# Optimization experiments

Measured on AMD Instinct MI355X. Metric: run time of the kernel, lower is better.

The kernel has to match this reference:

```python
import jax, jax.numpy as jnp
import numpy as np

B, H, SQ, SKV, D, TOPK = 1, 16, 1024, 4096, 128, 64


def setup_inputs() -> dict:
    key = jax.random.key(0)
    kq, kk, kv, ki, ks = jax.random.split(key, 5)
    q = jax.random.normal(kq, (B, H, SQ, D), dtype=jnp.float32)
    k = jax.random.normal(kk, (B, H, SKV, D), dtype=jnp.float32)
    v = jax.random.normal(kv, (B, H, SKV, D), dtype=jnp.float32)
    topk_indices = jax.random.randint(ki, (B, SQ, TOPK), 0, SKV, dtype=jnp.int32)
    topk_scores = jax.random.uniform(ks, (B, SQ, TOPK), dtype=jnp.float32)
    return {"q": q, "k": k, "v": v, "topk_indices": topk_indices,
            "topk_scores": topk_scores}


def reference(q, k, v, topk_indices, topk_scores):
    # q: (b,h,s,d); k,v: (b,h,S,d) global (cp_world_size=1 all-gather is identity)
    head_dim = q.shape[-1]
    scale = head_dim ** -0.5
    # Gather selected K/V per query without dense (b,h,s,S,d) expansion.
    # idx: (b,1,s,topk,1) broadcast against (b,h,1,S,d) along axis=3.
    idx = topk_indices[:, None, :, :, None]
    k_g = jnp.take_along_axis(k[:, :, None, :, :], idx, axis=3)  # (b,h,s,t,d)
    v_g = jnp.take_along_axis(v[:, :, None, :, :], idx, axis=3)  # (b,h,s,t,d)
    scores = jnp.einsum("bhsd,bhstd->bhst", q, k_g) * scale
    w = jax.nn.softmax(scores, axis=-1)
    # rescale by indexer scores and renormalize
    w = w * topk_scores[:, None, :, :]
    w = w / (jnp.sum(w, axis=-1, keepdims=True) + 1e-12)
    out = jnp.einsum("bhst,bhstd->bhsd", w, v_g)
    return out
```

## Files before the change

### kernel.cpp

```cpp
#include <hip/hip_runtime.h>
#include <hip/hip_fp16.h>

#define NH  16
#define SQL 1024
#define SKV 4096
#define HD  128
#define TK  64

typedef _Float16 h2_t __attribute__((ext_vector_type(2)));

__device__ __forceinline__ unsigned pkh(float x, float y) {
    return (unsigned)__half_as_ushort(__float2half(x)) |
           ((unsigned)__half_as_ushort(__float2half(y)) << 16);
}

__global__ __launch_bounds__(256) void cvt_f16(
    const float* __restrict__ k, const float* __restrict__ v,
    unsigned short* __restrict__ kh, unsigned short* __restrict__ vh)
{
    int b = blockIdx.x;
    const float* src; unsigned short* dst;
    if (b < 4096) { src = k; dst = kh; }
    else          { src = v; dst = vh; b -= 4096; }
    const size_t i = (size_t)b * 256 + threadIdx.x;
    const float4* s4 = (const float4*)src;
    float4 a = s4[2 * i], c = s4[2 * i + 1];
    uint4 o;
    o.x = pkh(a.x, a.y);
    o.y = pkh(a.z, a.w);
    o.z = pkh(c.x, c.y);
    o.w = pkh(c.z, c.w);
    ((uint4*)dst)[i] = o;
}

__global__ __launch_bounds__(256) void dsa_f16(
    const float* __restrict__ q, const unsigned short* __restrict__ kh,
    const unsigned short* __restrict__ vh, const int* __restrict__ tidx,
    const float* __restrict__ tsc, float* __restrict__ out)
{
    __shared__ int   idxs[4][TK];
    __shared__ float wsc[4][TK];
    __shared__ float scr[4][TK][17];

    const int tid  = threadIdx.x;
    const int wv   = tid >> 6;
    const int lane = tid & 63;
    const int quad = lane >> 4;
    const int l16  = lane & 15;
    const int bi   = blockIdx.x;

    const int h = ((bi >> 11) << 3) | (bi & 7);
    const int s = (((bi >> 3) & 255) << 2) + wv;

    const float* qp = q + (size_t)(h * SQL + s) * HD + 8 * l16;
    const float4 qa = *(const float4*)qp;
    const float4 qb = *(const float4*)(qp + 4);
    h2_t q0 = {(_Float16)qa.x, (_Float16)qa.y};
    h2_t q1 = {(_Float16)qa.z, (_Float16)qa.w};
    h2_t q2 = {(_Float16)qb.x, (_Float16)qb.y};
    h2_t q3 = {(_Float16)qb.z, (_Float16)qb.w};

    idxs[wv][lane] = tidx[s * TK + lane];
    const float t_sc = tsc[s * TK + lane];

    const unsigned short* kb = kh + (size_t)h * SKV * HD;
    float part[16];
#pragma unroll
    for (int i = 0; i < 16; ++i) {
        const int t   = 4 * i + quad;
        const size_t row = (size_t)idxs[wv][t];
        uint4 kw = *(const uint4*)(kb + row * HD + 8 * l16);
        float d = 0.f;
#if __has_builtin(__builtin_amdgcn_fdot2)
        d = __builtin_amdgcn_fdot2(q0, __builtin_bit_cast(h2_t, kw.x), d, false);
        d = __builtin_amdgcn_fdot2(q1, __builtin_bit_cast(h2_t, kw.y), d, false);
        d = __builtin_amdgcn_fdot2(q2, __builtin_bit_cast(h2_t, kw.z), d, false);
        d = __builtin_amdgcn_fdot2(q3, __builtin_bit_cast(h2_t, kw.w), d, false);
#else
        {
            float2 k0 = __half22float2(__builtin_bit_cast(__half2, kw.x));
            float2 k1 = __half22float2(__builtin_bit_cast(__half2, kw.y));
            float2 k2 = __half22float2(__builtin_bit_cast(__half2, kw.z));
            float2 k3 = __half22float2(__builtin_bit_cast(__half2, kw.w));
            d  = qa.x * k0.x + qa.y * k0.y + qa.z * k1.x + qa.w * k1.y;
            d += qb.x * k2.x + qb.y * k2.y + qb.z * k3.x + qb.w * k3.y;
        }
#endif
        part[i] = d;
    }

#pragma unroll
    for (int i = 0; i < 16; ++i) scr[wv][4 * i + quad][l16] = part[i];
    float acc = 0.f;
#pragma unroll
    for (int m = 0; m < 16; ++m) acc += scr[wv][lane][m];
    acc *= 0.08838834764831845f;

    float m = acc;
#pragma unroll
    for (int off = 32; off; off >>= 1) m = fmaxf(m, __shfl_xor(m, off));
    const float e   = __expf(acc - m);
    const float ets = e * t_sc;
    float se = e, sets = ets;
#pragma unroll
    for (int off = 32; off; off >>= 1) {
        se   += __shfl_xor(se, off);
        sets += __shfl_xor(sets, off);
    }
    wsc[wv][lane] = ets / (sets + 1e-12f * se);

    const unsigned short* vb = vh + (size_t)h * SKV * HD;
    __half2 o0 = __float2half2_rn(0.f);
    __half2 o1 = o0, o2 = o0, o3 = o0;
#pragma unroll 8
    for (int i = 0; i < TK / 4; ++i) {
        const int t    = 4 * i + quad;
        const size_t row = (size_t)idxs[wv][t];
        const __half2 w2 = __float2half2_rn(wsc[wv][t]);
        uint4 vw = *(const uint4*)(vb + row * HD + 8 * l16);
        o0 = __hfma2(w2, __builtin_bit_cast(__half2, vw.x), o0);
        o1 = __hfma2(w2, __builtin_bit_cast(__half2, vw.y), o1);
        o2 = __hfma2(w2, __builtin_bit_cast(__half2, vw.z), o2);
        o3 = __hfma2(w2, __builtin_bit_cast(__half2, vw.w), o3);
    }

    __half2 oo[4] = {o0, o1, o2, o3};
#pragma unroll
    for (int j = 0; j < 4; ++j) {
        unsigned u = __builtin_bit_cast(unsigned, oo[j]);
        oo[j] = __hadd2(oo[j], __builtin_bit_cast(__half2, __shfl_xor(u, 16)));
        u = __builtin_bit_cast(unsigned, oo[j]);
        oo[j] = __hadd2(oo[j], __builtin_bit_cast(__half2, __shfl_xor(u, 32)));
    }

    if (quad == 0) {
        float2 f0 = __half22float2(oo[0]);
        float2 f1 = __half22float2(oo[1]);
        float2 f2 = __half22float2(oo[2]);
        float2 f3 = __half22float2(oo[3]);
        float* op = out + (size_t)(h * SQL + s) * HD + 8 * l16;
        *(float4*)op       = make_float4(f0.x, f0.y, f1.x, f1.y);
        *(float4*)(op + 4) = make_float4(f2.x, f2.y, f3.x, f3.y);
    }
}

__global__ __launch_bounds__(256) void dsa_fp32(
    const float* __restrict__ q, const float* __restrict__ k,
    const float* __restrict__ v, const int* __restrict__ tidx,
    const float* __restrict__ tsc, float* __restrict__ out)
{
    __shared__ int   idxs[4][TK];
    __shared__ float wsc[4][TK];
    const int tid = threadIdx.x, wv = tid >> 6, lane = tid & 63;
    const int half = lane >> 5, l32 = lane & 31, bi = blockIdx.x;
    const int h = ((bi & 7) << 1) | ((bi >> 3) & 1);
    const int s = ((bi >> 4) << 2) + wv;
    const float* qp = q + (size_t)(h * SQL + s) * HD;
    const float4 qf = *(const float4*)(qp + 4 * l32);
    const float t_sc = tsc[s * TK + lane];
    idxs[wv][lane] = tidx[s * TK + lane];
    const float* kb = k + (size_t)h * SKV * HD;
#pragma unroll 4
    for (int i = 0; i < TK / 2; ++i) {
        const int t = 2 * i + half, row = idxs[wv][t];
        float4 k4 = *(const float4*)(kb + (size_t)row * HD + 4 * l32);
        float d = k4.x * qf.x + k4.y * qf.y + k4.z * qf.z + k4.w * qf.w;
        d += __shfl_xor(d, 16); d += __shfl_xor(d, 8); d += __shfl_xor(d, 4);
        d += __shfl_xor(d, 2);  d += __shfl_xor(d, 1);
        if (l32 == 0) wsc[wv][t] = d;
    }
    float acc = wsc[wv][lane] * 0.08838834764831845f;
    float m = acc;
#pragma unroll
    for (int off = 32; off; off >>= 1) m = fmaxf(m, __shfl_xor(m, off));
    const float e = __expf(acc - m), ets = e * t_sc;
    float se = e, sets = ets;
#pragma unroll
    for (int off = 32; off; off >>= 1) { se += __shfl_xor(se, off); sets += __shfl_xor(sets, off); }
    wsc[wv][lane] = ets / (sets + 1e-12f * se);
    const float* vbp = v + (size_t)h * SKV * HD;
    float4 o = make_float4(0.f, 0.f, 0.f, 0.f);
#pragma unroll 4
    for (int i = 0; i < TK / 2; ++i) {
        const int t = 2 * i + half, row = idxs[wv][t];
        const float wt = wsc[wv][t];
        float4 v4 = *(const float4*)(vbp + (size_t)row * HD + 4 * l32);
        o.x += wt * v4.x; o.y += wt * v4.y; o.z += wt * v4.z; o.w += wt * v4.w;
    }
    o.x += __shfl_xor(o.x, 32); o.y += __shfl_xor(o.y, 32);
    o.z += __shfl_xor(o.z, 32); o.w += __shfl_xor(o.w, 32);
    if (half == 0) *(float4*)(out + (size_t)(h * SQL + s) * HD + 4 * l32) = o;
}

extern "C" void kernel_launch(void* const* d_in, const int* in_sizes, int n_in,
                              void* d_out, int out_size, void* d_ws, size_t ws_size,
                              hipStream_t stream) {
    const float* q  = (const float*)d_in[0];
    const float* k  = (const float*)d_in[1];
    const float* v  = (const float*)d_in[2];
    const int*   ti = (const int*)d_in[3];
    const float* ts = (const float*)d_in[4];
    float* out = (float*)d_out;

    const size_t nkv  = (size_t)NH * SKV * HD;
    const size_t need = 2 * nkv * sizeof(unsigned short);
    if (ws_size >= need) {
        unsigned short* kh = (unsigned short*)d_ws;
        unsigned short* vh = kh + nkv;
        cvt_f16<<<dim3(8192), dim3(256), 0, stream>>>(k, v, kh, vh);
        dsa_f16<<<dim3(4096), dim3(256), 0, stream>>>(q, kh, vh, ti, ts, out);
    } else {
        dsa_fp32<<<dim3(4096), dim3(256), 0, stream>>>(q, k, v, ti, ts, out);
    }
}
```

Baseline: 133.6 us.

## Prefetch V rows before softmax and broadcast indices/weights via shuffles

Replaces the shared-memory index and weight arrays with wave shuffles (__shfl) of per-lane registers. Issues all 16 V-row gathers into registers right after the K dot products, so V loads overlap the score reduction and softmax instead of waiting on them. This raises register pressure (64 extra VGPRs for vw) and could lower occupancy.

Result: no change. 134.1 us, median of 2 (+0.4%).

```diff
diff --git a/kernel.cpp b/kernel.cpp
--- a/kernel.cpp
+++ b/kernel.cpp
@@ -38,8 +38,6 @@
     const unsigned short* __restrict__ vh, const int* __restrict__ tidx,
     const float* __restrict__ tsc, float* __restrict__ out)
 {
-    __shared__ int   idxs[4][TK];
-    __shared__ float wsc[4][TK];
     __shared__ float scr[4][TK][17];
 
     const int tid  = threadIdx.x;
@@ -60,15 +58,14 @@
     h2_t q2 = {(_Float16)qb.x, (_Float16)qb.y};
     h2_t q3 = {(_Float16)qb.z, (_Float16)qb.w};
 
-    idxs[wv][lane] = tidx[s * TK + lane];
-    const float t_sc = tsc[s * TK + lane];
+    const int   t_idx = tidx[s * TK + lane];
+    const float t_sc  = tsc[s * TK + lane];
 
     const unsigned short* kb = kh + (size_t)h * SKV * HD;
     float part[16];
 #pragma unroll
     for (int i = 0; i < 16; ++i) {
-        const int t   = 4 * i + quad;
-        const size_t row = (size_t)idxs[wv][t];
+        const size_t row = (size_t)__shfl(t_idx, 4 * i + quad);
         uint4 kw = *(const uint4*)(kb + row * HD + 8 * l16);
         float d = 0.f;
 #if __has_builtin(__builtin_amdgcn_fdot2)
@@ -89,6 +86,14 @@
         part[i] = d;
     }
 
+    const unsigned short* vb = vh + (size_t)h * SKV * HD;
+    uint4 vw[16];
+#pragma unroll
+    for (int i = 0; i < 16; ++i) {
+        const size_t row = (size_t)__shfl(t_idx, 4 * i + quad);
+        vw[i] = *(const uint4*)(vb + row * HD + 8 * l16);
+    }
+
 #pragma unroll
     for (int i = 0; i < 16; ++i) scr[wv][4 * i + quad][l16] = part[i];
     float acc = 0.f;
@@ -107,21 +112,18 @@
         se   += __shfl_xor(se, off);
         sets += __shfl_xor(sets, off);
     }
-    wsc[wv][lane] = ets / (sets + 1e-12f * se);
-
-    const unsigned short* vb = vh + (size_t)h * SKV * HD;
+    const float w = ets / (sets + 1e-12f * se);
+    const unsigned wpk = __builtin_bit_cast(unsigned, __float2half2_rn(w));
+
     __half2 o0 = __float2half2_rn(0.f);
     __half2 o1 = o0, o2 = o0, o3 = o0;
-#pragma unroll 8
-    for (int i = 0; i < TK / 4; ++i) {
-        const int t    = 4 * i + quad;
-        const size_t row = (size_t)idxs[wv][t];
-        const __half2 w2 = __float2half2_rn(wsc[wv][t]);
-        uint4 vw = *(const uint4*)(vb + row * HD + 8 * l16);
-        o0 = __hfma2(w2, __builtin_bit_cast(__half2, vw.x), o0);
-        o1 = __hfma2(w2, __builtin_bit_cast(__half2, vw.y), o1);
-        o2 = __hfma2(w2, __builtin_bit_cast(__half2, vw.z), o2);
-        o3 = __hfma2(w2, __builtin_bit_cast(__half2, vw.w), o3);
+#pragma unroll
+    for (int i = 0; i < 16; ++i) {
+        const __half2 w2 = __builtin_bit_cast(__half2, __shfl(wpk, 4 * i + quad));
+        o0 = __hfma2(w2, __builtin_bit_cast(__half2, vw[i].x), o0);
+        o1 = __hfma2(w2, __builtin_bit_cast(__half2, vw[i].y), o1);
+        o2 = __hfma2(w2, __builtin_bit_cast(__half2, vw[i].z), o2);
+        o3 = __hfma2(w2, __builtin_bit_cast(__half2, vw[i].w), o3);
     }
 
     __half2 oo[4] = {o0, o1, o2, o3};
```
